# Kernel tuning notes

Measured on AMD Instinct MI355X. Metric: run time of the kernel, lower is better.

## Reference

```python
import jax, jax.numpy as jnp
import numpy as np

HID = 64      # hidden_size of message MLP
NF = 20       # n_node_features
EF = 20       # n_edge_features
ITERS = 3
N_ENV, N_NODES, N_EDGES = 16, 5000, 50000


def setup_inputs() -> dict:
    key = jax.random.key(0)
    ks = jax.random.split(key, 12)
    s = 0.1
    node_features = jax.random.normal(ks[0], (N_ENV, N_NODES, NF), jnp.float32)
    edges = jax.random.randint(ks[1], (2, N_EDGES), 0, N_NODES, dtype=jnp.int32)
    # msg_net: Linear(2*NF,HID) -> Tanh -> Linear(HID,HID) -> Tanh -> Linear(HID,EF)
    W1 = jax.random.normal(ks[2], (HID, 2 * NF), jnp.float32) * s
    b1 = jax.random.normal(ks[3], (HID,), jnp.float32) * s
    W2 = jax.random.normal(ks[4], (HID, HID), jnp.float32) * s
    b2 = jax.random.normal(ks[5], (HID,), jnp.float32) * s
    W3 = jax.random.normal(ks[6], (EF, HID), jnp.float32) * s
    b3 = jax.random.normal(ks[7], (EF,), jnp.float32) * s
    # GRU(input=EF, hidden=NF): weight_ih (3*NF, EF), weight_hh (3*NF, NF)
    Wih = jax.random.normal(ks[8], (3 * NF, EF), jnp.float32) * s
    Whh = jax.random.normal(ks[9], (3 * NF, NF), jnp.float32) * s
    b_ih = jax.random.normal(ks[10], (3 * NF,), jnp.float32) * s
    b_hh = jax.random.normal(ks[11], (3 * NF,), jnp.float32) * s
    return {"node_features": node_features, "edges": edges,
            "W1": W1, "b1": b1, "W2": W2, "b2": b2, "W3": W3, "b3": b3,
            "Wih": Wih, "Whh": Whh, "b_ih": b_ih, "b_hh": b_hh}


def reference(node_features, edges, W1, b1, W2, b2, W3, b3, Wih, Whh, b_ih, b_hh):
    n_env, n_nodes, _ = node_features.shape
    # Bidirectionalize edges: cat([edges, edges[[1,0]]], dim=1)
    e = jnp.concatenate([edges, edges[::-1]], axis=1)  # (2, 2E)
    src, dst = e[0], e[1]
    for _ in range(ITERS):
        # gather src/dst node feats -> message MLP
        x = jnp.concatenate([node_features[:, src], node_features[:, dst]], axis=2)  # (env, 2E, 2*NF)
        h = jnp.tanh(x @ W1.T + b1)
        h = jnp.tanh(h @ W2.T + b2)
        msg = h @ W3.T + b3  # (env, 2E, EF)
        # scatter-add messages to source nodes
        store = jnp.zeros((n_env, n_nodes, EF), node_features.dtype).at[:, src].add(msg)
        # single-step GRU update (seq_len=1, h0=node_features), vectorized over env & node
        gi = store @ Wih.T + b_ih           # (env, nodes, 3*NF)
        gh = node_features @ Whh.T + b_hh   # (env, nodes, 3*NF)
        ir, iz, in_ = jnp.split(gi, 3, axis=-1)
        hr, hz, hn = jnp.split(gh, 3, axis=-1)
        r = jax.nn.sigmoid(ir + hr)
        z = jax.nn.sigmoid(iz + hz)
        n = jnp.tanh(in_ + r * hn)
        node_features = (1.0 - z) * n + z * node_features
    return node_features
```

## Files before the change

kernel.cpp:

```cpp
#include <hip/hip_runtime.h>

#define NFEAT 20
#define EFEAT 20
#define HID   64
#define NENV  16
#define NNODES 5000
#define NEDGES 50000
#define E2 (2*NEDGES)
#define ITERS 3
#define ROWS 64
#define THREADS 128
#define NPAD 24
#define CHUNKS ((E2 + ROWS - 1) / ROWS)

typedef __attribute__((ext_vector_type(8))) _Float16 f16x8;
typedef __attribute__((ext_vector_type(2))) __fp16  h16x2;
typedef __attribute__((ext_vector_type(4))) float f32x4;

__device__ __forceinline__ ushort f2h(float f) {
    _Float16 h = (_Float16)f;
    return *(ushort*)&h;
}
__device__ __forceinline__ unsigned pk2h(float a, float b) {
    h16x2 p = __builtin_amdgcn_cvt_pkrtz(a, b);
    return *(unsigned*)&p;
}
__device__ __forceinline__ float fast_tanh(float x) {
    float e = __builtin_exp2f(x * 2.8853900817779268f);
    float r = __builtin_amdgcn_rcpf(e + 1.f);
    return fmaf(-2.f, r, 1.f);
}
__device__ __forceinline__ float fast_sigmoid(float x) {
    float e = __builtin_exp2f(x * -1.4426950408889634f);
    return __builtin_amdgcn_rcpf(1.f + e);
}

__global__ __launch_bounds__(256) void hist_kernel(const int* __restrict__ edges,
                                                   int* __restrict__ cnt) {
    int e = blockIdx.x * 256 + threadIdx.x;
    if (e < E2) atomicAdd(&cnt[edges[e]], 1);
}

__global__ __launch_bounds__(256) void scan_kernel(const int* __restrict__ cnt,
                                                   int* __restrict__ cursor) {
    __shared__ int part[256];
    int t = threadIdx.x;
    int local[20]; int s = 0;
    int base = t * 20;
    #pragma unroll
    for (int i = 0; i < 20; i++) {
        int idx = base + i;
        int v = (idx < NNODES) ? cnt[idx] : 0;
        local[i] = s; s += v;
    }
    part[t] = s;
    __syncthreads();
    for (int d = 1; d < 256; d <<= 1) {
        int v = (t >= d) ? part[t - d] : 0;
        __syncthreads();
        part[t] += v;
        __syncthreads();
    }
    int excl = part[t] - s;
    #pragma unroll
    for (int i = 0; i < 20; i++) {
        int idx = base + i;
        if (idx < NNODES) cursor[idx] = excl + local[i];
    }
}

__global__ __launch_bounds__(256) void scatter_kernel(const int* __restrict__ edges,
                                                      int* __restrict__ cursor,
                                                      int* __restrict__ snode,
                                                      int* __restrict__ dnode) {
    int e = blockIdx.x * 256 + threadIdx.x;
    if (e < E2) {
        int s = edges[e];
        int di = e + NEDGES; if (di >= E2) di -= E2;
        int d = edges[di];
        int pos = atomicAdd(&cursor[s], 1);
        snode[pos] = s;
        dnode[pos] = d;
    }
}

__global__ void prep_weights(const float* __restrict__ W1, const float* __restrict__ W2,
                             const float* __restrict__ W3,
                             ushort* __restrict__ W1p, ushort* __restrict__ W2p,
                             ushort* __restrict__ W3p) {
    int t = threadIdx.x;
    for (int i = t; i < 64 * 64; i += 256) {
        int n = i >> 6, k = i & 63;
        float v = 0.f;
        if (k < NFEAT)                          v = W1[n * (2 * NFEAT) + k];
        else if (k >= NPAD && k < NPAD + NFEAT) v = W1[n * (2 * NFEAT) + NFEAT + (k - NPAD)];
        W1p[i] = f2h(v);
    }
    for (int i = t; i < 64 * 64; i += 256)
        W2p[i] = f2h(W2[i]);
    for (int i = t; i < 32 * 64; i += 256) {
        int n = i >> 6, k = i & 63;
        W3p[i] = (n < EFEAT) ? f2h(W3[n * HID + k]) : (ushort)0;
    }
}

__global__ __launch_bounds__(256) void conv_nf(const float* __restrict__ nf,
                                               ushort* __restrict__ nfp) {
    int gid = blockIdx.x * 256 + threadIdx.x;
    if (gid >= NENV * NNODES) return;
    const float* p = nf + (size_t)gid * NFEAT;
    ushort* ph = nfp + (size_t)gid * NPAD;
    #pragma unroll
    for (int k = 0; k < NFEAT; k++) ph[k] = f2h(p[k]);
    *(uint2*)(ph + NFEAT) = make_uint2(0u, 0u);
}

__global__ __launch_bounds__(THREADS) void edge_mlp_mfma(
    const ushort* __restrict__ nfp,
    const int*   __restrict__ snode, const int* __restrict__ dnode,
    const ushort* __restrict__ W1p, const ushort* __restrict__ W2p,
    const ushort* __restrict__ W3p,
    const float* __restrict__ b1, const float* __restrict__ b2,
    const float* __restrict__ b3,
    float* __restrict__ store)
{
    __shared__ ushort smem16[4096];
    ushort* Hp = smem16;
    float*  msgf = (float*)smem16;
    int*    msgi = (int*)smem16;

    const int tid   = threadIdx.x;
    const int wave  = tid >> 6;
    const int lane  = tid & 63;
    const int lr    = lane & 15;
    const int kg    = lane >> 4;
    const int m0    = wave * 32;
    const int env   = blockIdx.x & 15;
    const int chunk = blockIdx.x >> 4;
    const int base  = chunk * ROWS;
    const int envoff = env * NNODES;

#define MFMA2(acc, w0, w1, x0, x1)                                                  \
    acc = __builtin_amdgcn_mfma_f32_16x16x32_f16(w0, x0, acc, 0, 0, 0);             \
    acc = __builtin_amdgcn_mfma_f32_16x16x32_f16(w1, x1, acc, 0, 0, 0);

#define STORE_H4(accv, m_, rr_)                                                     \
    {                                                                               \
        float t0 = fast_tanh(accv[0]), t1 = fast_tanh(accv[1]);                     \
        float t2 = fast_tanh(accv[2]), t3 = fast_tanh(accv[3]);                     \
        unsigned p01 = pk2h(t0, t1), p23 = pk2h(t2, t3);                            \
        int c8 = (m_) * 2 + (kg >> 1);                                              \
        int idx = (rr_) * 64 + ((c8 ^ ((rr_) & 7)) << 3) + ((kg & 1) << 2);         \
        *(uint2*)(Hp + idx) = make_uint2(p01, p23);                                 \
    }

    {
        f16x8 wp[4][2];
        f32x4 bb[4];
        #pragma unroll
        for (int m = 0; m < 4; m++) {
            #pragma unroll
            for (int kt = 0; kt < 2; kt++)
                wp[m][kt] = *(const f16x8*)(W1p + (m * 16 + lr) * 64 + kt * 32 + kg * 8);
            bb[m] = *(const f32x4*)(b1 + m * 16 + kg * 4);
        }
        #pragma unroll
        for (int n = 0; n < 2; n++) {
            int rr = m0 + n * 16 + lr;
            int sr = base + rr;
            if (sr >= E2) sr = E2 - 1;
            const ushort* sp_ = nfp + (size_t)(envoff + snode[sr]) * NPAD;
            const ushort* dp_ = nfp + (size_t)(envoff + dnode[sr]) * NPAD;
            f16x8 x0, x1;
            if (kg < 3) x0 = *(const f16x8*)(sp_ + kg * 8);
            else        x0 = *(const f16x8*)(dp_);
            if (kg < 2) x1 = *(const f16x8*)(dp_ + 8 + kg * 8);
            else        x1 = f16x8{(_Float16)0,(_Float16)0,(_Float16)0,(_Float16)0,
                                   (_Float16)0,(_Float16)0,(_Float16)0,(_Float16)0};
            f32x4 acc[4];
            #pragma unroll
            for (int m = 0; m < 4; m++) {
                acc[m] = bb[m];
                MFMA2(acc[m], wp[m][0], wp[m][1], x0, x1)
            }
            #pragma unroll
            for (int m = 0; m < 4; m++) STORE_H4(acc[m], m, rr)
        }
    }

    {
        f16x8 wp[4][2];
        f32x4 bb[4];
        #pragma unroll
        for (int m = 0; m < 4; m++) {
            #pragma unroll
            for (int kt = 0; kt < 2; kt++)
                wp[m][kt] = *(const f16x8*)(W2p + (m * 16 + lr) * 64 + kt * 32 + kg * 8);
            bb[m] = *(const f32x4*)(b2 + m * 16 + kg * 4);
        }
        #pragma unroll
        for (int n = 0; n < 2; n++) {
            int rr = m0 + n * 16 + lr, sw = rr & 7;
            f16x8 x0 = *(const f16x8*)(Hp + rr * 64 + ((kg ^ sw) << 3));
            f16x8 x1 = *(const f16x8*)(Hp + rr * 64 + (((4 + kg) ^ sw) << 3));
            f32x4 acc[4];
            #pragma unroll
            for (int m = 0; m < 4; m++) {
                acc[m] = bb[m];
                MFMA2(acc[m], wp[m][0], wp[m][1], x0, x1)
            }
            #pragma unroll
            for (int m = 0; m < 4; m++) STORE_H4(acc[m], m, rr)
        }
    }

    {
        int i_ = lane & 31;
        int sr_i = base + m0 + i_;
        int key  = (sr_i < E2) ? (envoff + snode[sr_i]) : -1;

        f16x8 w3[2][2];
        #pragma unroll
        for (int m = 0; m < 2; m++)
            #pragma unroll
            for (int kt = 0; kt < 2; kt++)
                w3[m][kt] = *(const f16x8*)(W3p + (m * 16 + lr) * 64 + kt * 32 + kg * 8);
        f32x4 bb0 = *(const f32x4*)(b3 + kg * 4);
        f32x4 bb1 = (kg == 0) ? *(const f32x4*)(b3 + 16)
                              : f32x4{0.f, 0.f, 0.f, 0.f};

        f16x8 xb[2][2];
        #pragma unroll
        for (int n = 0; n < 2; n++) {
            int rr = m0 + n * 16 + lr, sw = rr & 7;
            xb[n][0] = *(const f16x8*)(Hp + rr * 64 + ((kg ^ sw) << 3));
            xb[n][1] = *(const f16x8*)(Hp + rr * 64 + (((4 + kg) ^ sw) << 3));
        }
        f32x4 acc0[2], acc1[2];
        #pragma unroll
        for (int n = 0; n < 2; n++) {
            acc0[n] = bb0;
            MFMA2(acc0[n], w3[0][0], w3[0][1], xb[n][0], xb[n][1])
            acc1[n] = bb1;
            MFMA2(acc1[n], w3[1][0], w3[1][1], xb[n][0], xb[n][1])
        }

        int wbase = wave * 1024;
        #pragma unroll
        for (int n = 0; n < 2; n++) {
            int row = n * 16 + lr;
            int g0 = kg ^ (row & 7);
            *(f32x4*)(msgf + wbase + row * 32 + (g0 << 2)) = acc0[n];
            if (kg == 0) {
                int g1 = 4 ^ (row & 7);
                *(f32x4*)(msgf + wbase + row * 32 + (g1 << 2)) = acc1[n];
            }
        }
        if (lane < 32) msgi[wbase + i_ * 32 + ((5 ^ (i_ & 7)) << 2)] = key;

        int nxt = __shfl_down(key, 1);
        bool flag = (i_ == 31) || (key != nxt);
        unsigned fm = (unsigned)__ballot(flag);

        if (lane < EFEAT) {
            int c = lane, g = c >> 2, o = c & 3;
            float sum = 0.f;
            for (int i = 0; i < 32; i++) {
                sum += msgf[wbase + i * 32 + ((g ^ (i & 7)) << 2) + o];
                if ((fm >> i) & 1u) {
                    int curk = msgi[wbase + i * 32 + ((5 ^ (i & 7)) << 2)];
                    if (curk >= 0)
                        atomicAdd(store + (size_t)curk * EFEAT + c, sum);
                    sum = 0.f;
                }
            }
        }
    }
#undef STORE_H4
#undef MFMA2
}

__global__ __launch_bounds__(256) void gru_kernel(
    float* __restrict__ store,
    const float* __restrict__ Wih, const float* __restrict__ bih,
    const float* __restrict__ Whh, const float* __restrict__ bhh,
    float* __restrict__ nf,
    ushort* __restrict__ nfp)
{
    int gid = blockIdx.x * blockDim.x + threadIdx.x;
    const int total = NENV * NNODES;
    if (gid >= total) return;

    float*       s = store + (size_t)gid * EFEAT;
    float*       h = nf    + (size_t)gid * NFEAT;
    ushort*     ph = nfp   + (size_t)gid * NPAD;

    float sv[EFEAT], hv[NFEAT];
    #pragma unroll
    for (int k = 0; k < EFEAT; k++) sv[k] = s[k];
    #pragma unroll
    for (int k = 0; k < NFEAT; k++) hv[k] = h[k];

    {
        float4 z = make_float4(0.f, 0.f, 0.f, 0.f);
        #pragma unroll
        for (int q = 0; q < 5; q++) *(float4*)(s + q * 4) = z;
    }

    for (int t = 0; t < NFEAT; t++) {
        float ir = bih[t],            hr = bhh[t];
        float iz = bih[NFEAT + t],    hz = bhh[NFEAT + t];
        float in_ = bih[2*NFEAT + t], hn = bhh[2*NFEAT + t];
        const float* wr = Wih + t * EFEAT;
        const float* wz = Wih + (NFEAT + t) * EFEAT;
        const float* wn = Wih + (2*NFEAT + t) * EFEAT;
        #pragma unroll
        for (int k = 0; k < EFEAT; k++) {
            ir  = fmaf(sv[k], wr[k], ir);
            iz  = fmaf(sv[k], wz[k], iz);
            in_ = fmaf(sv[k], wn[k], in_);
        }
        const float* vr = Whh + t * NFEAT;
        const float* vz = Whh + (NFEAT + t) * NFEAT;
        const float* vn = Whh + (2*NFEAT + t) * NFEAT;
        #pragma unroll
        for (int k = 0; k < NFEAT; k++) {
            hr = fmaf(hv[k], vr[k], hr);
            hz = fmaf(hv[k], vz[k], hz);
            hn = fmaf(hv[k], vn[k], hn);
        }
        float r = fast_sigmoid(ir + hr);
        float z = fast_sigmoid(iz + hz);
        float n = fast_tanh(in_ + r * hn);
        float hw = (1.f - z) * n + z * hv[t];
        h[t] = hw;
        ph[t] = f2h(hw);
    }
    *(uint2*)(ph + NFEAT) = make_uint2(0u, 0u);
}

extern "C" void kernel_launch(void* const* d_in, const int* in_sizes, int n_in,
                              void* d_out, int out_size, void* d_ws, size_t ws_size,
                              hipStream_t stream) {
    const float* nf_in = (const float*)d_in[0];
    const int*   edges = (const int*)d_in[1];
    const float* W1 = (const float*)d_in[2];
    const float* b1 = (const float*)d_in[3];
    const float* W2 = (const float*)d_in[4];
    const float* b2 = (const float*)d_in[5];
    const float* W3 = (const float*)d_in[6];
    const float* b3 = (const float*)d_in[7];
    const float* Wih = (const float*)d_in[8];
    const float* Whh = (const float*)d_in[9];
    const float* bih = (const float*)d_in[10];
    const float* bhh = (const float*)d_in[11];

    float* nf    = (float*)d_out;
    float* store = (float*)d_ws;
    const size_t nf_bytes    = (size_t)NENV * NNODES * NFEAT * sizeof(float);
    const size_t store_bytes = (size_t)NENV * NNODES * EFEAT * sizeof(float);
    ushort* W1p = (ushort*)((char*)d_ws + store_bytes);
    ushort* W2p = W1p + 64 * 64;
    ushort* W3p = W2p + 64 * 64;
    ushort* nfp = W3p + 32 * 64;
    int* cnt    = (int*)(nfp + (size_t)NENV * NNODES * NPAD);
    int* cursor = cnt + NNODES;
    int* snode  = cursor + NNODES;
    int* dnode  = snode + E2;

    prep_weights<<<1, 256, 0, stream>>>(W1, W2, W3, W1p, W2p, W3p);
    conv_nf<<<(NENV * NNODES + 255) / 256, 256, 0, stream>>>(nf_in, nfp);
    hipMemcpyAsync(nf, nf_in, nf_bytes, hipMemcpyDeviceToDevice, stream);
    hipMemsetAsync(cnt, 0, NNODES * sizeof(int), stream);
    hipMemsetAsync(store, 0, store_bytes, stream);
    hist_kernel<<<(E2 + 255) / 256, 256, 0, stream>>>(edges, cnt);
    scan_kernel<<<1, 256, 0, stream>>>(cnt, cursor);
    scatter_kernel<<<(E2 + 255) / 256, 256, 0, stream>>>(edges, cursor, snode, dnode);

    const int edge_blocks = NENV * CHUNKS;
    dim3 grid_n((NENV * NNODES + 255) / 256);

    for (int it = 0; it < ITERS; it++) {
        edge_mlp_mfma<<<edge_blocks, THREADS, 0, stream>>>(nfp, snode, dnode,
                                                           W1p, W2p, W3p,
                                                           b1, b2, b3, store);
        gru_kernel<<<grid_n, 256, 0, stream>>>(store, Wih, bih, Whh, bhh, nf, nfp);
    }
}
```

Before: 576.7 us.

## Make edge MLP blocks persistent over four tiles with prefetched gathers

Edge MLP blocks grow to 256 threads and each processes four 128-edge tiles in a loop. All weights and biases are loaded into registers once per block, and the next tile's node-feature gather is issued before the layer-2 and layer-3 work of the current tile. The aim is to amortise weight loads and hide gather latency. The cost is much higher register pressure, larger shared memory and fewer blocks. The kernel has no barriers and each wave uses only its own shared-memory rows, so reusing them across iterations appears safe.

Measured after the change: 631.1 us. +9.4%, slower.

```diff
diff --git a/kernel.cpp b/kernel.cpp
--- a/kernel.cpp
+++ b/kernel.cpp
@@ -8,10 +8,12 @@
 #define NEDGES 50000
 #define E2 (2*NEDGES)
 #define ITERS 3
-#define ROWS 64
-#define THREADS 128
+#define TILE 128
+#define NCHUNK 4
+#define SPAN (TILE*NCHUNK)
+#define GRPS ((E2 + SPAN - 1) / SPAN)
+#define THREADS 256
 #define NPAD 24
-#define CHUNKS ((E2 + ROWS - 1) / ROWS)
 
 typedef __attribute__((ext_vector_type(8))) _Float16 f16x8;
 typedef __attribute__((ext_vector_type(2))) __fp16  h16x2;
@@ -124,7 +126,7 @@
     const float* __restrict__ b3,
     float* __restrict__ store)
 {
-    __shared__ ushort smem16[4096];
+    __shared__ ushort smem16[8192];
     ushort* Hp = smem16;
     float*  msgf = (float*)smem16;
     int*    msgi = (int*)smem16;
@@ -134,10 +136,10 @@
     const int lane  = tid & 63;
     const int lr    = lane & 15;
     const int kg    = lane >> 4;
+    const int i_    = lane & 31;
     const int m0    = wave * 32;
     const int env   = blockIdx.x & 15;
-    const int chunk = blockIdx.x >> 4;
-    const int base  = chunk * ROWS;
+    const int grp   = blockIdx.x >> 4;
     const int envoff = env * NNODES;
 
 #define MFMA2(acc, w0, w1, x0, x1)                                                  \
@@ -154,128 +156,165 @@
         *(uint2*)(Hp + idx) = make_uint2(p01, p23);                                 \
     }
 
+#define LOADX(x0_, x1_, sn_, dn_)                                                   \
+    {                                                                               \
+        const ushort* sp_ = nfp + (size_t)(envoff + (sn_)) * NPAD;                  \
+        const ushort* dp_ = nfp + (size_t)(envoff + (dn_)) * NPAD;                  \
+        if (kg < 3) x0_ = *(const f16x8*)(sp_ + kg * 8);                            \
+        else        x0_ = *(const f16x8*)(dp_);                                     \
+        if (kg < 2) x1_ = *(const f16x8*)(dp_ + 8 + kg * 8);                        \
+        else        x1_ = f16x8{(_Float16)0,(_Float16)0,(_Float16)0,(_Float16)0,    \
+                                (_Float16)0,(_Float16)0,(_Float16)0,(_Float16)0};   \
+    }
+
+    f16x8 wp1[4][2], wp2[4][2], w3[2][2];
+    f32x4 bb1v[4], bb2v[4];
+    #pragma unroll
+    for (int m = 0; m < 4; m++) {
+        #pragma unroll
+        for (int kt = 0; kt < 2; kt++) {
+            wp1[m][kt] = *(const f16x8*)(W1p + (m * 16 + lr) * 64 + kt * 32 + kg * 8);
+            wp2[m][kt] = *(const f16x8*)(W2p + (m * 16 + lr) * 64 + kt * 32 + kg * 8);
+        }
+        bb1v[m] = *(const f32x4*)(b1 + m * 16 + kg * 4);
+        bb2v[m] = *(const f32x4*)(b2 + m * 16 + kg * 4);
+    }
+    #pragma unroll
+    for (int m = 0; m < 2; m++)
+        #pragma unroll
+        for (int kt = 0; kt < 2; kt++)
+            w3[m][kt] = *(const f16x8*)(W3p + (m * 16 + lr) * 64 + kt * 32 + kg * 8);
+    const f32x4 bb30 = *(const f32x4*)(b3 + kg * 4);
+    const f32x4 bb31 = (kg == 0) ? *(const f32x4*)(b3 + 16) : f32x4{0.f,0.f,0.f,0.f};
+
+    int srA = grp * SPAN + m0 + lr;
+    int srB = srA + 16;
+    int srK = grp * SPAN + m0 + i_;
+    f16x8 xa0, xa1, xb0, xb1;
+    int key;
     {
-        f16x8 wp[4][2];
-        f32x4 bb[4];
-        #pragma unroll
-        for (int m = 0; m < 4; m++) {
-            #pragma unroll
-            for (int kt = 0; kt < 2; kt++)
-                wp[m][kt] = *(const f16x8*)(W1p + (m * 16 + lr) * 64 + kt * 32 + kg * 8);
-            bb[m] = *(const f32x4*)(b1 + m * 16 + kg * 4);
-        }
-        #pragma unroll
-        for (int n = 0; n < 2; n++) {
-            int rr = m0 + n * 16 + lr;
-            int sr = base + rr;
-            if (sr >= E2) sr = E2 - 1;
-            const ushort* sp_ = nfp + (size_t)(envoff + snode[sr]) * NPAD;
-            const ushort* dp_ = nfp + (size_t)(envoff + dnode[sr]) * NPAD;
-            f16x8 x0, x1;
-            if (kg < 3) x0 = *(const f16x8*)(sp_ + kg * 8);
-            else        x0 = *(const f16x8*)(dp_);
-            if (kg < 2) x1 = *(const f16x8*)(dp_ + 8 + kg * 8);
-            else        x1 = f16x8{(_Float16)0,(_Float16)0,(_Float16)0,(_Float16)0,
-                                   (_Float16)0,(_Float16)0,(_Float16)0,(_Float16)0};
+        int a = (srA < E2) ? srA : (E2 - 1);
+        int b = (srB < E2) ? srB : (E2 - 1);
+        int snA = snode[a], dnA = dnode[a];
+        int snB = snode[b], dnB = dnode[b];
+        key = (srK < E2) ? (envoff + snode[srK]) : -1;
+        LOADX(xa0, xa1, snA, dnA)
+        LOADX(xb0, xb1, snB, dnB)
+    }
+
+    for (int it = 0; it < NCHUNK; ++it) {
+        const int rrA = m0 + lr;
+        const int rrB = m0 + 16 + lr;
+
+        {
             f32x4 acc[4];
             #pragma unroll
             for (int m = 0; m < 4; m++) {
-                acc[m] = bb[m];
-                MFMA2(acc[m], wp[m][0], wp[m][1], x0, x1)
-            }
-            #pragma unroll
-            for (int m = 0; m < 4; m++) STORE_H4(acc[m], m, rr)
-        }
-    }
-
-    {
-        f16x8 wp[4][2];
-        f32x4 bb[4];
-        #pragma unroll
-        for (int m = 0; m < 4; m++) {
-            #pragma unroll
-            for (int kt = 0; kt < 2; kt++)
-                wp[m][kt] = *(const f16x8*)(W2p + (m * 16 + lr) * 64 + kt * 32 + kg * 8);
-            bb[m] = *(const f32x4*)(b2 + m * 16 + kg * 4);
-        }
-        #pragma unroll
-        for (int n = 0; n < 2; n++) {
-            int rr = m0 + n * 16 + lr, sw = rr & 7;
-            f16x8 x0 = *(const f16x8*)(Hp + rr * 64 + ((kg ^ sw) << 3));
-            f16x8 x1 = *(const f16x8*)(Hp + rr * 64 + (((4 + kg) ^ sw) << 3));
+                acc[m] = bb1v[m];
+                MFMA2(acc[m], wp1[m][0], wp1[m][1], xa0, xa1)
+            }
+            #pragma unroll
+            for (int m = 0; m < 4; m++) STORE_H4(acc[m], m, rrA)
+            #pragma unroll
+            for (int m = 0; m < 4; m++) {
+                acc[m] = bb1v[m];
+                MFMA2(acc[m], wp1[m][0], wp1[m][1], xb0, xb1)
+            }
+            #pragma unroll
+            for (int m = 0; m < 4; m++) STORE_H4(acc[m], m, rrB)
+        }
+
+        f16x8 nxa0, nxa1, nxb0, nxb1;
+        int nkey = -1;
+        if (it + 1 < NCHUNK) {
+            srA += TILE; srB += TILE; srK += TILE;
+            int a = (srA < E2) ? srA : (E2 - 1);
+            int b = (srB < E2) ? srB : (E2 - 1);
+            int snA = snode[a], dnA = dnode[a];
+            int snB = snode[b], dnB = dnode[b];
+            nkey = (srK < E2) ? (envoff + snode[srK]) : -1;
+            LOADX(nxa0, nxa1, snA, dnA)
+            LOADX(nxb0, nxb1, snB, dnB)
+        }
+
+        {
+            int swA = rrA & 7, swB = rrB & 7;
+            f16x8 h0A = *(const f16x8*)(Hp + rrA * 64 + ((kg ^ swA) << 3));
+            f16x8 h1A = *(const f16x8*)(Hp + rrA * 64 + (((4 + kg) ^ swA) << 3));
+            f16x8 h0B = *(const f16x8*)(Hp + rrB * 64 + ((kg ^ swB) << 3));
+            f16x8 h1B = *(const f16x8*)(Hp + rrB * 64 + (((4 + kg) ^ swB) << 3));
             f32x4 acc[4];
             #pragma unroll
             for (int m = 0; m < 4; m++) {
-                acc[m] = bb[m];
-                MFMA2(acc[m], wp[m][0], wp[m][1], x0, x1)
-            }
-            #pragma unroll
-            for (int m = 0; m < 4; m++) STORE_H4(acc[m], m, rr)
-        }
-    }
-
-    {
-        int i_ = lane & 31;
-        int sr_i = base + m0 + i_;
-        int key  = (sr_i < E2) ? (envoff + snode[sr_i]) : -1;
-
-        f16x8 w3[2][2];
-        #pragma unroll
-        for (int m = 0; m < 2; m++)
-            #pragma unroll
-            for (int kt = 0; kt < 2; kt++)
-                w3[m][kt] = *(const f16x8*)(W3p + (m * 16 + lr) * 64 + kt * 32 + kg * 8);
-        f32x4 bb0 = *(const f32x4*)(b3 + kg * 4);
-        f32x4 bb1 = (kg == 0) ? *(const f32x4*)(b3 + 16)
-                              : f32x4{0.f, 0.f, 0.f, 0.f};
-
-        f16x8 xb[2][2];
-        #pragma unroll
-        for (int n = 0; n < 2; n++) {
-            int rr = m0 + n * 16 + lr, sw = rr & 7;
-            xb[n][0] = *(const f16x8*)(Hp + rr * 64 + ((kg ^ sw) << 3));
-            xb[n][1] = *(const f16x8*)(Hp + rr * 64 + (((4 + kg) ^ sw) << 3));
-        }
-        f32x4 acc0[2], acc1[2];
-        #pragma unroll
-        for (int n = 0; n < 2; n++) {
-            acc0[n] = bb0;
-            MFMA2(acc0[n], w3[0][0], w3[0][1], xb[n][0], xb[n][1])
-            acc1[n] = bb1;
-            MFMA2(acc1[n], w3[1][0], w3[1][1], xb[n][0], xb[n][1])
-        }
-
-        int wbase = wave * 1024;
-        #pragma unroll
-        for (int n = 0; n < 2; n++) {
-            int row = n * 16 + lr;
-            int g0 = kg ^ (row & 7);
-            *(f32x4*)(msgf + wbase + row * 32 + (g0 << 2)) = acc0[n];
-            if (kg == 0) {
-                int g1 = 4 ^ (row & 7);
-                *(f32x4*)(msgf + wbase + row * 32 + (g1 << 2)) = acc1[n];
-            }
-        }
-        if (lane < 32) msgi[wbase + i_ * 32 + ((5 ^ (i_ & 7)) << 2)] = key;
-
-        int nxt = __shfl_down(key, 1);
-        bool flag = (i_ == 31) || (key != nxt);
-        unsigned fm = (unsigned)__ballot(flag);
-
-        if (lane < EFEAT) {
-            int c = lane, g = c >> 2, o = c & 3;
-            float sum = 0.f;
-            for (int i = 0; i < 32; i++) {
-                sum += msgf[wbase + i * 32 + ((g ^ (i & 7)) << 2) + o];
-                if ((fm >> i) & 1u) {
-                    int curk = msgi[wbase + i * 32 + ((5 ^ (i & 7)) << 2)];
-                    if (curk >= 0)
-                        atomicAdd(store + (size_t)curk * EFEAT + c, sum);
-                    sum = 0.f;
+                acc[m] = bb2v[m];
+                MFMA2(acc[m], wp2[m][0], wp2[m][1], h0A, h1A)
+            }
+            #pragma unroll
+            for (int m = 0; m < 4; m++) STORE_H4(acc[m], m, rrA)
+            #pragma unroll
+            for (int m = 0; m < 4; m++) {
+                acc[m] = bb2v[m];
+                MFMA2(acc[m], wp2[m][0], wp2[m][1], h0B, h1B)
+            }
+            #pragma unroll
+            for (int m = 0; m < 4; m++) STORE_H4(acc[m], m, rrB)
+        }
+
+        {
+            int swA = rrA & 7, swB = rrB & 7;
+            f16x8 h0A = *(const f16x8*)(Hp + rrA * 64 + ((kg ^ swA) << 3));
+            f16x8 h1A = *(const f16x8*)(Hp + rrA * 64 + (((4 + kg) ^ swA) << 3));
+            f16x8 h0B = *(const f16x8*)(Hp + rrB * 64 + ((kg ^ swB) << 3));
+            f16x8 h1B = *(const f16x8*)(Hp + rrB * 64 + (((4 + kg) ^ swB) << 3));
+            f32x4 acc0A = bb30, acc1A = bb31, acc0B = bb30, acc1B = bb31;
+            MFMA2(acc0A, w3[0][0], w3[0][1], h0A, h1A)
+            MFMA2(acc1A, w3[1][0], w3[1][1], h0A, h1A)
+            MFMA2(acc0B, w3[0][0], w3[0][1], h0B, h1B)
+            MFMA2(acc1B, w3[1][0], w3[1][1], h0B, h1B)
+
+            int wbase = wave * 1024;
+            {
+                int rowA = lr;
+                int g0 = kg ^ (rowA & 7);
+                *(f32x4*)(msgf + wbase + rowA * 32 + (g0 << 2)) = acc0A;
+                if (kg == 0) {
+                    int g1 = 4 ^ (rowA & 7);
+                    *(f32x4*)(msgf + wbase + rowA * 32 + (g1 << 2)) = acc1A;
                 }
-            }
-        }
-    }
+                int rowB = 16 + lr;
+                int g0b = kg ^ (rowB & 7);
+                *(f32x4*)(msgf + wbase + rowB * 32 + (g0b << 2)) = acc0B;
+                if (kg == 0) {
+                    int g1b = 4 ^ (rowB & 7);
+                    *(f32x4*)(msgf + wbase + rowB * 32 + (g1b << 2)) = acc1B;
+                }
+            }
+            if (lane < 32) msgi[wbase + i_ * 32 + ((5 ^ (i_ & 7)) << 2)] = key;
+
+            int nxt = __shfl_down(key, 1);
+            bool flag = (i_ == 31) || (key != nxt);
+            unsigned fm = (unsigned)__ballot(flag);
+
+            if (lane < EFEAT) {
+                int c = lane, g = c >> 2, o = c & 3;
+                float sum = 0.f;
+                for (int i = 0; i < 32; i++) {
+                    sum += msgf[wbase + i * 32 + ((g ^ (i & 7)) << 2) + o];
+                    if ((fm >> i) & 1u) {
+                        int curk = msgi[wbase + i * 32 + ((5 ^ (i & 7)) << 2)];
+                        if (curk >= 0)
+                            atomicAdd(store + (size_t)curk * EFEAT + c, sum);
+                        sum = 0.f;
+                    }
+                }
+            }
+        }
+
+        if (it + 1 < NCHUNK) {
+            xa0 = nxa0; xa1 = nxa1; xb0 = nxb0; xb1 = nxb1; key = nkey;
+        }
+    }
+#undef LOADX
 #undef STORE_H4
 #undef MFMA2
 }
@@ -377,7 +416,7 @@
     scan_kernel<<<1, 256, 0, stream>>>(cnt, cursor);
     scatter_kernel<<<(E2 + 255) / 256, 256, 0, stream>>>(edges, cursor, snode, dnode);
 
-    const int edge_blocks = NENV * CHUNKS;
+    const int edge_blocks = NENV * GRPS;
     dim3 grid_n((NENV * NNODES + 255) / 256);
 
     for (int it = 0; it < ITERS; it++) {
```
